# Performance work log

Hardware: AMD Instinct MI355X
Metric: run time of the kernel (lower is better)

## Reference

```python
import jax, jax.numpy as jnp
import numpy as np

B, S, D, H = 2, 2048, 1024, 16
DK = D // H  # 64


def setup_inputs() -> dict:
    key = jax.random.key(0)
    ks = jax.random.split(key, 10)
    query = jax.random.normal(ks[0], (B, S, D), dtype=jnp.float32)
    key_t = jax.random.normal(ks[1], (B, S, D), dtype=jnp.float32)
    value = jax.random.normal(ks[2], (B, S, D), dtype=jnp.float32)
    # binary mask [batch, q_size, k_size]: causal lower-triangular, same per batch
    mask = jnp.broadcast_to(jnp.tril(jnp.ones((S, S), dtype=jnp.float32)), (B, S, S))
    sc = 0.02
    Wq = jax.random.normal(ks[3], (D, D), dtype=jnp.float32) * sc
    bq = jnp.zeros((D,), dtype=jnp.float32)
    Wk = jax.random.normal(ks[4], (D, D), dtype=jnp.float32) * sc
    bk = jnp.zeros((D,), dtype=jnp.float32)
    Wv = jax.random.normal(ks[5], (D, D), dtype=jnp.float32) * sc
    bv = jnp.zeros((D,), dtype=jnp.float32)
    return {"query": query, "key": key_t, "value": value, "mask": mask,
            "Wq": Wq, "bq": bq, "Wk": Wk, "bk": bk, "Wv": Wv, "bv": bv}


def reference(query, key, value, mask, Wq, bq, Wk, bk, Wv, bv):
    # ReLU-activated Q/K/V projections (Dense(..., activation='relu'))
    Q = jax.nn.relu(query @ Wq + bq)   # [B, Sq, D]
    K = jax.nn.relu(key @ Wk + bk)     # [B, Sk, D]
    V = jax.nn.relu(value @ Wv + bv)   # [B, Sk, D]
    b, sq, _ = Q.shape
    sk = K.shape[1]
    # split-concat head trick == reshape last dim into (H, DK) heads
    Qh = Q.reshape(b, sq, H, DK)
    Kh = K.reshape(b, sk, H, DK)
    Vh = V.reshape(b, sk, H, DK)
    scores = jnp.einsum('bqhd,bkhd->bhqk', Qh, Kh) / jnp.sqrt(jnp.float32(DK))
    m = mask[:, None, :, :]  # broadcast over heads (mask_expander tiles over h)
    scores = scores * m + (1.0 - m) * (-1e10)
    attn = jax.nn.softmax(scores, axis=-1)  # dropout is a no-op (see notes)
    out = jnp.einsum('bhqk,bkhd->bqhd', attn, Vh).reshape(b, sq, H * DK)
    return out
```

## Files before the change

kernel.cpp:

```cpp
#include <hip/hip_runtime.h>
#include <hip/hip_bf16.h>

#define B_  2
#define S_  2048
#define D_  1024
#define H_  16
#define DK_ 64
#define NR  (B_*S_)
#define QT_ 16
#define CPP 20

typedef __bf16 bf16_t;
typedef __attribute__((ext_vector_type(8)))  __bf16 bf16x8;
typedef __attribute__((ext_vector_type(4)))  float  f32x4;
typedef __attribute__((ext_vector_type(16))) float  f32x16;

#define QSCALE (0.125f * 1.44269504088896340736f)

__device__ inline void gl_lds16(const void* g, void* l) {
  __builtin_amdgcn_global_load_lds(
      (const __attribute__((address_space(1))) void*)g,
      (__attribute__((address_space(3))) void*)l, 16, 0, 0);
}

__device__ inline unsigned pack2(float a, float b) {
  union { bf16_t h[2]; unsigned u; } x;
  x.h[0] = (bf16_t)a; x.h[1] = (bf16_t)b;
  return x.u;
}

__device__ inline float fast_exp2(float x) {
  float r;
  asm("v_exp_f32 %0, %1" : "=v"(r) : "v"(x));
  return r;
}

__device__ inline bf16x8 frag(const bf16_t* p, int r, int j) {
  return *(const bf16x8*)(p + r * 64 + ((j ^ (r & 7)) * 8));
}
__device__ inline bf16x8 frag32(const bf16_t* p, int r, int j) {
  return *(const bf16x8*)(p + r * 32 + ((j ^ ((r >> 1) & 3)) * 8));
}

__device__ const unsigned char ord_p[CPP] = {7,6,5,4,3,2,7,6,5,4,7,6,1,7,5,3,6,4,2,0};
__device__ const unsigned char ord_c[CPP] = {0,0,0,0,0,0,1,1,1,1,2,2,0,3,2,1,3,2,1,0};
__device__ const unsigned char cbase[8]   = {0,1,2,4,6,9,12,16};

__global__ void transpose_cvt(const float* __restrict__ wq, const float* __restrict__ wk,
                              const float* __restrict__ wv,
                              bf16_t* __restrict__ oq, bf16_t* __restrict__ ok,
                              bf16_t* __restrict__ ov) {
  const int z = blockIdx.z;
  const float* W = z == 0 ? wq : z == 1 ? wk : wv;
  bf16_t*     WT = z == 0 ? oq : z == 1 ? ok : ov;
  __shared__ float t[32][33];
  int x  = blockIdx.x * 32 + threadIdx.x;
  int y0 = blockIdx.y * 32;
  for (int i = threadIdx.y; i < 32; i += 8)
    t[i][threadIdx.x] = W[(size_t)(y0 + i) * D_ + x];
  __syncthreads();
  int k  = y0 + threadIdx.x;
  int n0 = blockIdx.x * 32;
  for (int i = threadIdx.y; i < 32; i += 8)
    WT[(size_t)(n0 + i) * D_ + k] = (bf16_t)t[threadIdx.x][i];
}

struct AReg { float4 a[4]; };

__global__ __launch_bounds__(256, 3) void gemm_qkv(
    const float* __restrict__ XFq, const float* __restrict__ XFk, const float* __restrict__ XFv,
    const bf16_t* __restrict__ Wq, const bf16_t* __restrict__ Wk, const bf16_t* __restrict__ Wv,
    const float* __restrict__ bq, const float* __restrict__ bk, const float* __restrict__ bv,
    bf16_t* __restrict__ Yq, bf16_t* __restrict__ Yk, bf16_t* __restrict__ Yv)
{
  const int z = blockIdx.z;
  const float*  XF   = z == 0 ? XFq : z == 1 ? XFk : XFv;
  const bf16_t* WT   = z == 0 ? Wq : z == 1 ? Wk : Wv;
  const float*  bias = z == 0 ? bq : z == 1 ? bk : bv;
  bf16_t*       Y    = z == 0 ? Yq : z == 1 ? Yk : Yv;
  const float scale  = z == 0 ? QSCALE : 1.0f;
  const int transposedV = (z == 2);

  __shared__ bf16_t As[3][128 * 32];
  __shared__ bf16_t Bs[3][128 * 32];
  const int m0 = blockIdx.x * 128, n0 = blockIdx.y * 128;
  const int t = threadIdx.x, l = t & 63, w = t >> 6;
  const int wm = (w & 1) * 64, wn = (w >> 1) * 64;
  const int lr = l & 15, lg4 = l >> 4;

  f32x4 acc[4][4] = {};

  auto loadA = [&](int k0) {
    AReg r;
    #pragma unroll
    for (int i = 0; i < 2; i++) {
      int c = i * 256 + t;
      int row = c >> 2, j = c & 3;
      const float* src = XF + (size_t)(m0 + row) * D_ + k0 + j * 8;
      r.a[2 * i]     = *(const float4*)src;
      r.a[2 * i + 1] = *(const float4*)(src + 4);
    }
    return r;
  };
  auto cvtWriteA = [&](int bi, const AReg& r) {
    #pragma unroll
    for (int i = 0; i < 2; i++) {
      int c = i * 256 + t;
      int row = c >> 2, j = c & 3;
      union { bf16_t h[8]; bf16x8 v; } pk;
      #pragma unroll
      for (int k = 0; k < 4; k++) {
        pk.h[k]     = (bf16_t)r.a[2 * i][k];
        pk.h[4 + k] = (bf16_t)r.a[2 * i + 1][k];
      }
      *(bf16x8*)&As[bi][row * 32 + ((j ^ ((row >> 1) & 3)) * 8)] = pk.v;
    }
  };
  auto stageB = [&](int bi, int k0) {
    #pragma unroll
    for (int i = 0; i < 2; i++) {
      int c = i * 256 + t;
      int row = c >> 2, j = c & 3;
      int sc = (j ^ ((row >> 1) & 3)) * 8;
      gl_lds16(WT + (size_t)(n0 + row) * D_ + k0 + sc, &Bs[bi][c * 8]);
    }
  };

  AReg aA = loadA(0);
  stageB(0, 0);
  AReg aNext = loadA(32);
  stageB(1, 32);
  cvtWriteA(0, aA);
  asm volatile("s_waitcnt vmcnt(6) lgkmcnt(0)" ::: "memory");
  __builtin_amdgcn_s_barrier();
  __builtin_amdgcn_sched_barrier(0);

  const int NSTEP = D_ / 32;
  for (int p = 0; p < NSTEP; ++p) {
    const int cur = p - (p / 3) * 3;

    AReg aNew;
    const bool more = (p + 2 < NSTEP);
    if (more) {
      const int nb = (p + 2) - ((p + 2) / 3) * 3;
      aNew = loadA((p + 2) * 32);
      stageB(nb, (p + 2) * 32);
    }

    bf16x8 af[4], bfr[4];
    #pragma unroll
    for (int mf = 0; mf < 4; mf++)
      af[mf] = frag32(&As[cur][0], wm + mf * 16 + lr, lg4);
    #pragma unroll
    for (int nf = 0; nf < 4; nf++)
      bfr[nf] = frag32(&Bs[cur][0], wn + nf * 16 + lr, lg4);
    __builtin_amdgcn_s_setprio(1);
    #pragma unroll
    for (int mf = 0; mf < 4; mf++)
      #pragma unroll
      for (int nf = 0; nf < 4; nf++)
        acc[mf][nf] = __builtin_amdgcn_mfma_f32_16x16x32_bf16(
            af[mf], bfr[nf], acc[mf][nf], 0, 0, 0);
    __builtin_amdgcn_s_setprio(0);

    if (p + 1 < NSTEP) {
      const int nb1 = (p + 1) - ((p + 1) / 3) * 3;
      cvtWriteA(nb1, aNext);
      if (more) asm volatile("s_waitcnt vmcnt(6) lgkmcnt(0)" ::: "memory");
      else      asm volatile("s_waitcnt vmcnt(0) lgkmcnt(0)" ::: "memory");
      __builtin_amdgcn_s_barrier();
      __builtin_amdgcn_sched_barrier(0);
      aNext = aNew;
    }
  }

  #pragma unroll
  for (int nf = 0; nf < 4; nf++) {
    int col = n0 + wn + nf * 16 + lr;
    float bvv = bias[col];
    #pragma unroll
    for (int mf = 0; mf < 4; mf++) {
      if (!transposedV) {
        #pragma unroll
        for (int r = 0; r < 4; r++) {
          int row = m0 + wm + mf * 16 + lg4 * 4 + r;
          float v = fmaxf(acc[mf][nf][r] + bvv, 0.f) * scale;
          Y[(size_t)row * D_ + col] = (bf16_t)v;
        }
      } else {
        int row0 = m0 + wm + mf * 16 + lg4 * 4;
        int bb = row0 >> 11, s0 = row0 & (S_ - 1);
        int hh = col >> 6,  dk = col & (DK_ - 1);
        union { bf16_t h[4]; unsigned long long u; } pk;
        #pragma unroll
        for (int r = 0; r < 4; r++)
          pk.h[r] = (bf16_t)fmaxf(acc[mf][nf][r] + bvv, 0.f);
        *(unsigned long long*)&Y[(((size_t)(bb * H_ + hh)) * DK_ + dk) * S_ + s0] = pk.u;
      }
    }
  }
}

__device__ inline void qkt(const bf16_t* kl, const bf16x8* qf, int lq, int hh,
                           f32x16& s0, f32x16& s1) {
  #pragma unroll
  for (int s = 0; s < 4; s++) {
    bf16x8 k0 = frag(kl, lq, 2 * s + hh);
    bf16x8 k1 = frag(kl, lq + 32, 2 * s + hh);
    s0 = __builtin_amdgcn_mfma_f32_32x32x16_bf16(k0, qf[s], s0, 0, 0, 0);
    s1 = __builtin_amdgcn_mfma_f32_32x32x16_bf16(k1, qf[s], s1, 0, 0, 0);
  }
}

__device__ inline void cmask(f32x16& s0, f32x16& s1, int kb, int q, int hh) {
  #pragma unroll
  for (int r = 0; r < 16; r++) {
    int krow = kb + (r & 3) + 8 * (r >> 2) + 4 * hh;
    if (krow > q)      s0[r] = -1e30f;
    if (krow + 32 > q) s1[r] = -1e30f;
  }
}

__device__ inline void pv_quad(const f32x16& p0, const f32x16& p1,
                               const bf16_t* vl, int lq, int hh,
                               f32x16& o0, f32x16& o1) {
  #pragma unroll
  for (int st = 0; st < 4; st++) {
    const f32x16& ps = (st < 2) ? p0 : p1;
    const int bb = (st & 1) * 8;
    unsigned lo0 = pack2(ps[bb + 0], ps[bb + 1]), lo1 = pack2(ps[bb + 2], ps[bb + 3]);
    unsigned hi0 = pack2(ps[bb + 4], ps[bb + 5]), hi1 = pack2(ps[bb + 6], ps[bb + 7]);
    unsigned sA = hh ? lo0 : hi0, sB = hh ? lo1 : hi1;
    unsigned rA = __shfl_xor(sA, 32, 64), rB = __shfl_xor(sB, 32, 64);
    union { unsigned u[4]; bf16x8 v; } pf;
    pf.u[0] = hh ? rA : lo0;  pf.u[1] = hh ? rB : lo1;
    pf.u[2] = hh ? hi0 : rA;  pf.u[3] = hh ? hi1 : rB;
    bf16x8 v0 = frag(vl, lq, 2 * st + hh);
    bf16x8 v1 = frag(vl, lq + 32, 2 * st + hh);
    o0 = __builtin_amdgcn_mfma_f32_32x32x16_bf16(v0, pf.v, o0, 0, 0, 0);
    o1 = __builtin_amdgcn_mfma_f32_32x32x16_bf16(v1, pf.v, o1, 0, 0, 0);
  }
}

__global__ __launch_bounds__(512, 4) void attn_fwd(
    const bf16_t* __restrict__ Q, const bf16_t* __restrict__ K,
    const bf16_t* __restrict__ VT, bf16_t* __restrict__ PO,
    float* __restrict__ PL)
{
  __shared__ bf16_t lbuf[3][8192];

  const int bx = blockIdx.x;
  const int unit = bx >> 5, bh = bx & 31;
  const int p_ = ord_p[unit], ch = ord_c[unit];
  const int b = bh >> 4, h = bh & 15;
  const int kt0 = ch * 8;
  const int nt = min(8, (4 * p_ + 4) - kt0);
  const int slotbase = (bh * CPP + cbase[p_] + ch) * 2;

  const int t = threadIdx.x, w = t >> 6, l = t & 63;
  const int u = w >> 2, w4 = w & 3;
  const int qt = 2 * p_ + u;
  const int q0 = qt * 128 + w4 * 32;
  const int lq = l & 31, hh = l >> 5;
  const int qq = q0 + lq;
  const int nfull = 2 * qt + (w4 >> 1);

  const bf16_t* Qb = Q  + ((size_t)(b * S_ + qq)) * D_ + h * DK_;
  const bf16_t* Kb = K  + ((size_t)b * S_) * D_ + h * DK_;
  const bf16_t* Vb = VT + ((size_t)(b * H_ + h)) * ((size_t)DK_ * S_);

  const int r0 = t >> 3, j0 = t & 7;
  const int jx = (j0 ^ (r0 & 7)) * 8;

  #define STAGE_TILE(bi, kt_) do {                                    \
    const int kb_ = (kt_) << 6;                                       \
    bf16_t* Lb = lbuf[bi];                                            \
    gl_lds16(Kb + (size_t)(kb_ + r0) * D_ + jx, Lb + t * 8);          \
    gl_lds16(Vb + (size_t)r0 * S_ + kb_ + jx,   Lb + 4096 + t * 8);   \
  } while (0)

  bf16x8 qf[4];
  #pragma unroll
  for (int s = 0; s < 4; s++)
    qf[s] = *(const bf16x8*)(Qb + s * 16 + hh * 8);
  asm volatile("s_waitcnt vmcnt(0)" ::: "memory");
  #pragma unroll
  for (int s = 0; s < 4; s++)
    asm volatile("" : "+v"(qf[s]));

  f32x16 o0 = {}, o1 = {};
  f32x16 lacc = {};

  STAGE_TILE(0, kt0);
  STAGE_TILE(1, kt0 + 1);
  asm volatile("s_waitcnt vmcnt(2)" ::: "memory");
  __builtin_amdgcn_s_barrier();
  __builtin_amdgcn_sched_barrier(0);

  for (int p = 0; p < nt; ++p) {
    const int kt = kt0 + p;
    const int cur = p - (p / 3) * 3;

    if (p + 2 < nt) {
      const int nb = (p + 2) - ((p + 2) / 3) * 3;
      STAGE_TILE(nb, kt + 2);
    }

    if (kt <= nfull) {
      const bf16_t* kl = lbuf[cur];
      const bf16_t* vl = lbuf[cur] + 4096;

      f32x16 s0 = {}, s1 = {};
      __builtin_amdgcn_s_setprio(1);
      qkt(kl, qf, lq, hh, s0, s1);
      __builtin_amdgcn_s_setprio(0);
      if (kt == nfull) cmask(s0, s1, kt << 6, qq, hh);

      f32x16 p0, p1;
      #pragma unroll
      for (int r2 = 0; r2 < 16; r2++) {
        p0[r2] = fast_exp2(s0[r2]);
        p1[r2] = fast_exp2(s1[r2]);
        lacc[r2] += p0[r2] + p1[r2];
      }

      __builtin_amdgcn_s_setprio(1);
      pv_quad(p0, p1, vl, lq, hh, o0, o1);
      __builtin_amdgcn_s_setprio(0);
    }

    if (p + 1 < nt) {
      if (p + 2 < nt) asm volatile("s_waitcnt vmcnt(2)" ::: "memory");
      else            asm volatile("s_waitcnt vmcnt(0)" ::: "memory");
      __builtin_amdgcn_s_barrier();
      __builtin_amdgcn_sched_barrier(0);
    }
  }
  #undef STAGE_TILE

  float lrun = 0.f;
  #pragma unroll
  for (int r2 = 0; r2 < 16; r2++) lrun += lacc[r2];
  lrun += __shfl_xor(lrun, 32, 64);

  bf16_t* po = PO + (size_t)(slotbase + u) * 8192;
  #pragma unroll
  for (int r2 = 0; r2 < 16; r2++) {
    int dk = (r2 & 3) + 8 * (r2 >> 2) + 4 * hh;
    po[dk * 128 + w4 * 32 + lq]        = (bf16_t)o0[r2];
    po[(dk + 32) * 128 + w4 * 32 + lq] = (bf16_t)o1[r2];
  }
  if (hh == 0)
    PL[(size_t)(slotbase + u) * 128 + w4 * 32 + lq] = lrun;
}

__global__ __launch_bounds__(256, 4) void attn_combine(
    const bf16_t* __restrict__ PO, const float* __restrict__ PL,
    float* __restrict__ out)
{
  const int bx = blockIdx.x;
  const int b = bx >> 8, h = (bx >> 4) & 15, qt = bx & 15;
  const int bh = b * H_ + h;
  const int p_ = qt >> 1, u = qt & 1;
  const int nc = (p_ >> 1) + 1;
  const int slot0 = (bh * CPP + cbase[p_]) * 2 + u;

  __shared__ float ls[64][132];
  __shared__ float inv[128];

  const int t = threadIdx.x;

  float acc[4][8];
  #pragma unroll
  for (int i = 0; i < 4; i++)
    #pragma unroll
    for (int j = 0; j < 8; j++) acc[i][j] = 0.f;

  for (int c = 0; c < nc; ++c) {
    const bf16_t* po = PO + (size_t)(slot0 + 2 * c) * 8192;
    #pragma unroll
    for (int i = 0; i < 4; i++) {
      bf16x8 v = *(const bf16x8*)(po + i * 2048 + t * 8);
      #pragma unroll
      for (int j = 0; j < 8; j++) acc[i][j] += (float)v[j];
    }
  }

  if (t < 128) {
    float s = 0.f;
    for (int c = 0; c < nc; ++c) s += PL[(size_t)(slot0 + 2 * c) * 128 + t];
    inv[t] = 1.0f / s;
  }

  #pragma unroll
  for (int i = 0; i < 4; i++)
    #pragma unroll
    for (int j = 0; j < 8; j++)
      ls[(t >> 4) + 16 * i][(t & 15) * 8 + j] = acc[i][j];
  __syncthreads();

  const int q = t >> 1, c0 = (t & 1) * 32;
  const float iv = inv[q];
  float* op = out + ((size_t)(b * S_ + qt * 128 + q)) * D_ + h * DK_ + c0;
  #pragma unroll
  for (int v = 0; v < 8; v++) {
    float4 x = { ls[c0 + 4 * v][q] * iv,     ls[c0 + 4 * v + 1][q] * iv,
                 ls[c0 + 4 * v + 2][q] * iv, ls[c0 + 4 * v + 3][q] * iv };
    *(float4*)(op + 4 * v) = x;
  }
}

extern "C" void kernel_launch(void* const* d_in, const int* in_sizes, int n_in,
                              void* d_out, int out_size, void* d_ws, size_t ws_size,
                              hipStream_t stream) {
  const float* query = (const float*)d_in[0];
  const float* keyi  = (const float*)d_in[1];
  const float* val   = (const float*)d_in[2];
  const float* Wq = (const float*)d_in[4];
  const float* bq = (const float*)d_in[5];
  const float* Wk = (const float*)d_in[6];
  const float* bk = (const float*)d_in[7];
  const float* Wv = (const float*)d_in[8];
  const float* bv = (const float*)d_in[9];
  float* out = (float*)d_out;

  const size_t XB = (size_t)NR * D_;
  const size_t WB = (size_t)D_ * D_;
  bf16_t* ws  = (bf16_t*)d_ws;
  bf16_t* WTq = ws + 3 * XB;
  bf16_t* WTk = WTq + WB;
  bf16_t* WTv = WTk + WB;
  bf16_t* Qm  = WTv + WB;
  bf16_t* Km  = Qm  + XB;
  bf16_t* VTm = Km  + XB;
  bf16_t* PO  = ws;
  float*  PL  = (float*)((char*)d_ws + 22u * 1024 * 1024);

  dim3 tgrid(D_ / 32, D_ / 32, 3), tblk(32, 8);
  transpose_cvt<<<tgrid, tblk, 0, stream>>>(Wq, Wk, Wv, WTq, WTk, WTv);

  dim3 ggrid(NR / 128, D_ / 128, 3);
  gemm_qkv<<<ggrid, 256, 0, stream>>>(query, keyi, val, WTq, WTk, WTv,
                                      bq, bk, bv, Qm, Km, VTm);

  attn_fwd<<<dim3(32 * CPP), 512, 0, stream>>>(Qm, Km, VTm, PO, PL);
  attn_combine<<<dim3(B_ * H_ * QT_), 256, 0, stream>>>(PO, PL, out);
}
```

Measured before the change: 95.88 us.

## Double-buffer paired K/V tiles in attention forward to halve barrier count

The attention main loop now stages two 64-key K/V tiles per step into a double buffer, replacing the triple-buffered single-tile scheme. It then runs both QK^T blocks back to back before the two softmax-exp and PV stages. This halves the number of waitcnt and barrier synchronisations per block and raises the work done per barrier. In exchange, LDS per block grows from 48KB to 64KB and the launch-bounds occupancy hint drops from 4 to 2. Loads now wait for vmcnt(0) with only one stage of prefetch ahead, which may reduce how much load latency is hidden.

```diff
diff --git a/kernel.cpp b/kernel.cpp
--- a/kernel.cpp
+++ b/kernel.cpp
@@ -242,12 +242,12 @@
   }
 }
 
-__global__ __launch_bounds__(512, 4) void attn_fwd(
+__global__ __launch_bounds__(512, 2) void attn_fwd(
     const bf16_t* __restrict__ Q, const bf16_t* __restrict__ K,
     const bf16_t* __restrict__ VT, bf16_t* __restrict__ PO,
     float* __restrict__ PL)
 {
-  __shared__ bf16_t lbuf[3][8192];
+  __shared__ bf16_t lbuf[2][16384];
 
   const int bx = blockIdx.x;
   const int unit = bx >> 5, bh = bx & 31;
@@ -255,6 +255,7 @@
   const int b = bh >> 4, h = bh & 15;
   const int kt0 = ch * 8;
   const int nt = min(8, (4 * p_ + 4) - kt0);
+  const int np = nt >> 1;
   const int slotbase = (bh * CPP + cbase[p_] + ch) * 2;
 
   const int t = threadIdx.x, w = t >> 6, l = t & 63;
@@ -272,11 +273,13 @@
   const int r0 = t >> 3, j0 = t & 7;
   const int jx = (j0 ^ (r0 & 7)) * 8;
 
-  #define STAGE_TILE(bi, kt_) do {                                    \
-    const int kb_ = (kt_) << 6;                                       \
-    bf16_t* Lb = lbuf[bi];                                            \
-    gl_lds16(Kb + (size_t)(kb_ + r0) * D_ + jx, Lb + t * 8);          \
-    gl_lds16(Vb + (size_t)r0 * S_ + kb_ + jx,   Lb + 4096 + t * 8);   \
+  #define STAGE_PAIR(bi, kt_) do {                                        \
+    const int kb_ = (kt_) << 6;                                           \
+    bf16_t* Lb = lbuf[bi];                                                \
+    gl_lds16(Kb + (size_t)(kb_ + r0) * D_ + jx,      Lb + t * 8);         \
+    gl_lds16(Kb + (size_t)(kb_ + 64 + r0) * D_ + jx, Lb + 4096 + t * 8);  \
+    gl_lds16(Vb + (size_t)r0 * S_ + kb_ + jx,        Lb + 8192 + t * 8);  \
+    gl_lds16(Vb + (size_t)r0 * S_ + kb_ + 64 + jx,   Lb + 12288 + t * 8); \
   } while (0)
 
   bf16x8 qf[4];
@@ -291,52 +294,72 @@
   f32x16 o0 = {}, o1 = {};
   f32x16 lacc = {};
 
-  STAGE_TILE(0, kt0);
-  STAGE_TILE(1, kt0 + 1);
-  asm volatile("s_waitcnt vmcnt(2)" ::: "memory");
+  STAGE_PAIR(0, kt0);
+  asm volatile("s_waitcnt vmcnt(0)" ::: "memory");
   __builtin_amdgcn_s_barrier();
   __builtin_amdgcn_sched_barrier(0);
 
-  for (int p = 0; p < nt; ++p) {
-    const int kt = kt0 + p;
-    const int cur = p - (p / 3) * 3;
-
-    if (p + 2 < nt) {
-      const int nb = (p + 2) - ((p + 2) / 3) * 3;
-      STAGE_TILE(nb, kt + 2);
-    }
-
-    if (kt <= nfull) {
-      const bf16_t* kl = lbuf[cur];
-      const bf16_t* vl = lbuf[cur] + 4096;
-
-      f32x16 s0 = {}, s1 = {};
+  for (int p = 0; p < np; ++p) {
+    const int t0 = kt0 + 2 * p, t1 = t0 + 1;
+    const int cur = p & 1;
+
+    if (p + 1 < np) STAGE_PAIR(cur ^ 1, t0 + 2);
+
+    const bf16_t* base = lbuf[cur];
+    if (t1 <= nfull) {
+      f32x16 sa0 = {}, sa1 = {}, sb0 = {}, sb1 = {};
       __builtin_amdgcn_s_setprio(1);
-      qkt(kl, qf, lq, hh, s0, s1);
+      qkt(base,        qf, lq, hh, sa0, sa1);
+      qkt(base + 4096, qf, lq, hh, sb0, sb1);
       __builtin_amdgcn_s_setprio(0);
-      if (kt == nfull) cmask(s0, s1, kt << 6, qq, hh);
-
-      f32x16 p0, p1;
+      if (t1 == nfull) cmask(sb0, sb1, t1 << 6, qq, hh);
+
+      f32x16 pa0, pa1;
       #pragma unroll
       for (int r2 = 0; r2 < 16; r2++) {
-        p0[r2] = fast_exp2(s0[r2]);
-        p1[r2] = fast_exp2(s1[r2]);
-        lacc[r2] += p0[r2] + p1[r2];
+        pa0[r2] = fast_exp2(sa0[r2]);
+        pa1[r2] = fast_exp2(sa1[r2]);
+        lacc[r2] += pa0[r2] + pa1[r2];
       }
-
       __builtin_amdgcn_s_setprio(1);
-      pv_quad(p0, p1, vl, lq, hh, o0, o1);
+      pv_quad(pa0, pa1, base + 8192, lq, hh, o0, o1);
       __builtin_amdgcn_s_setprio(0);
-    }
-
-    if (p + 1 < nt) {
-      if (p + 2 < nt) asm volatile("s_waitcnt vmcnt(2)" ::: "memory");
-      else            asm volatile("s_waitcnt vmcnt(0)" ::: "memory");
+
+      f32x16 pb0, pb1;
+      #pragma unroll
+      for (int r2 = 0; r2 < 16; r2++) {
+        pb0[r2] = fast_exp2(sb0[r2]);
+        pb1[r2] = fast_exp2(sb1[r2]);
+        lacc[r2] += pb0[r2] + pb1[r2];
+      }
+      __builtin_amdgcn_s_setprio(1);
+      pv_quad(pb0, pb1, base + 12288, lq, hh, o0, o1);
+      __builtin_amdgcn_s_setprio(0);
+    } else if (t0 <= nfull) {
+      f32x16 sa0 = {}, sa1 = {};
+      __builtin_amdgcn_s_setprio(1);
+      qkt(base, qf, lq, hh, sa0, sa1);
+      __builtin_amdgcn_s_setprio(0);
+      cmask(sa0, sa1, t0 << 6, qq, hh);
+      f32x16 pa0, pa1;
+      #pragma unroll
+      for (int r2 = 0; r2 < 16; r2++) {
+        pa0[r2] = fast_exp2(sa0[r2]);
+        pa1[r2] = fast_exp2(sa1[r2]);
+        lacc[r2] += pa0[r2] + pa1[r2];
+      }
+      __builtin_amdgcn_s_setprio(1);
+      pv_quad(pa0, pa1, base + 8192, lq, hh, o0, o1);
+      __builtin_amdgcn_s_setprio(0);
+    }
+
+    if (p + 1 < np) {
+      asm volatile("s_waitcnt vmcnt(0)" ::: "memory");
       __builtin_amdgcn_s_barrier();
       __builtin_amdgcn_sched_barrier(0);
     }
   }
-  #undef STAGE_TILE
+  #undef STAGE_PAIR
 
   float lrun = 0.f;
   #pragma unroll
```

Result: no change. 95.51 us (median of 3 runs) (-0.4%).
